# Kernel tuning notes

Hardware: AMD Instinct MI355X
Metric: run time of the kernel (lower is better)

The kernel has to match this reference:

```python
import jax, jax.numpy as jnp
import numpy as np

N = 100000  # nodes
E = 1600000  # edges
D = 128     # hid_dim
LN_EPS = 1e-5


def setup_inputs() -> dict:
    key = jax.random.key(0)
    ks = jax.random.split(key, 14)
    s = 1.0 / np.sqrt(D)
    s2 = 1.0 / np.sqrt(2 * D)
    return {
        "x": jax.random.normal(ks[0], (N, D), jnp.float32),
        "ei": jax.random.randint(ks[1], (2, E), 0, N, dtype=jnp.int32),
        # gin1 mlp: Linear(D,D) + LayerNorm(D)
        "W1": jax.random.normal(ks[2], (D, D), jnp.float32) * s,
        "b1": jnp.zeros((D,), jnp.float32),
        "g1": jnp.ones((D,), jnp.float32),
        "bt1": jnp.zeros((D,), jnp.float32),
        # gin2 mlp
        "W2": jax.random.normal(ks[3], (D, D), jnp.float32) * s,
        "b2": jnp.zeros((D,), jnp.float32),
        "g2": jnp.ones((D,), jnp.float32),
        "bt2": jnp.zeros((D,), jnp.float32),
        # merge MLP: Linear(2D,2D) -> ReLU -> Linear(2D,D) -> ReLU
        "Wl1": jax.random.normal(ks[4], (2 * D, 2 * D), jnp.float32) * s2,
        "bl1": jnp.zeros((2 * D,), jnp.float32),
        "Wl2": jax.random.normal(ks[5], (D, 2 * D), jnp.float32) * s2,
        "bl2": jnp.zeros((D,), jnp.float32),
    }


def _layer_norm(h, g, b):
    mu = jnp.mean(h, axis=-1, keepdims=True)
    var = jnp.mean(jnp.square(h - mu), axis=-1, keepdims=True)
    return (h - mu) * jax.lax.rsqrt(var + LN_EPS) * g + b


def _gin_branch(x, src, dst, W, b, g, beta):
    # GINConv with eps=0: h = x + sum_{(src->dst)} x[src]
    agg = jax.ops.segment_sum(x[src], dst, num_segments=N)
    h = x + agg
    # ResBlock(Linear -> LayerNorm -> ReLU)
    y = jax.nn.relu(_layer_norm(h @ W.T + b, g, beta))
    return h + y


def reference(x, ei, W1, b1, g1, bt1, W2, b2, g2, bt2, Wl1, bl1, Wl2, bl2):
    src, dst = ei[0], ei[1]
    ret1 = _gin_branch(x, src, dst, W1, b1, g1, bt1)        # original edges
    ret2 = _gin_branch(x, dst, src, W2, b2, g2, bt2)        # flipped edges ei[[1,0]]
    cat = jnp.concatenate((ret1, ret2), axis=-1)            # [N, 2D]
    h = jax.nn.relu(cat @ Wl1.T + bl1)
    return jax.nn.relu(h @ Wl2.T + bl2)                     # [N, D]
```

## Files before the change

### kernel.cpp

```cpp
#include <hip/hip_runtime.h>
#include <hip/hip_bf16.h>

#define NN 100000
#define EE 1600000
#define DD 128
#define SCAN_N (2 * NN)
#define SCAN_BLOCKS ((SCAN_N + 1023) / 1024)
#define FILL_PASSES 4
#define FILL_RANGE (NN / FILL_PASSES)

__global__ __launch_bounds__(256) void k_transpose_all(const float* __restrict__ W1,
                                                       const float* __restrict__ W2,
                                                       const float* __restrict__ Wl1,
                                                       const float* __restrict__ Wl2,
                                                       float* __restrict__ Wt1,
                                                       float* __restrict__ Wt2,
                                                       float* __restrict__ Wtl1,
                                                       float* __restrict__ Wtl2) {
    int tid = blockIdx.x * 256 + threadIdx.x;
    const float* in;
    float* out;
    int C, R, off;
    if (tid < 16384)      { in = W1;  out = Wt1;  R = 128; C = 128; off = 0; }
    else if (tid < 32768) { in = W2;  out = Wt2;  R = 128; C = 128; off = 16384; }
    else if (tid < 98304) { in = Wl1; out = Wtl1; R = 256; C = 256; off = 32768; }
    else                  { in = Wl2; out = Wtl2; R = 128; C = 256; off = 98304; }
    int i = tid - off;
    int r = i / C, c = i - r * C;
    out[c * R + r] = in[i];
}

__global__ __launch_bounds__(256) void k_count(const int* __restrict__ ei,
                                               int* __restrict__ off) {
    int e = blockIdx.x * 256 + threadIdx.x;
    int s = ei[e];
    int d = ei[EE + e];
    atomicAdd(&off[d], 1);
    atomicAdd(&off[NN + s], 1);
}

__global__ __launch_bounds__(256) void k_scan1(int* __restrict__ off,
                                               int* __restrict__ bsum) {
    __shared__ int s[256];
    int t = threadIdx.x;
    int base = blockIdx.x * 1024 + t * 4;
    int v[4];
    #pragma unroll
    for (int i = 0; i < 4; ++i) {
        int g = base + i;
        v[i] = (g < SCAN_N) ? off[g] : 0;
    }
    int local = v[0] + v[1] + v[2] + v[3];
    s[t] = local;
    __syncthreads();
    #pragma unroll
    for (int o = 1; o < 256; o <<= 1) {
        int add = (t >= o) ? s[t - o] : 0;
        __syncthreads();
        s[t] += add;
        __syncthreads();
    }
    int run = s[t] - local;
    #pragma unroll
    for (int i = 0; i < 4; ++i) {
        int g = base + i;
        if (g < SCAN_N) off[g] = run;
        run += v[i];
    }
    if (t == 0) bsum[blockIdx.x] = s[255];
}

__global__ __launch_bounds__(256) void k_scan2(int* __restrict__ bsum) {
    __shared__ int s[256];
    int t = threadIdx.x;
    int local = (t < SCAN_BLOCKS) ? bsum[t] : 0;
    s[t] = local;
    __syncthreads();
    #pragma unroll
    for (int o = 1; o < 256; o <<= 1) {
        int add = (t >= o) ? s[t - o] : 0;
        __syncthreads();
        s[t] += add;
        __syncthreads();
    }
    if (t < SCAN_BLOCKS) bsum[t] = s[t] - local;
}

__global__ __launch_bounds__(256) void k_scan3(int* __restrict__ off,
                                               const int* __restrict__ bsum,
                                               int* __restrict__ cur) {
    int t = threadIdx.x;
    int base = blockIdx.x * 1024 + t * 4;
    int add = bsum[blockIdx.x];
    #pragma unroll
    for (int i = 0; i < 4; ++i) {
        int g = base + i;
        if (g < SCAN_N) {
            int v = off[g] + add;
            off[g] = v;
            cur[g] = v;
        }
    }
    if (blockIdx.x == 0 && t == 0) off[SCAN_N] = 2 * EE;
}

__global__ __launch_bounds__(256) void k_fill(const int* __restrict__ ei,
                                              int* __restrict__ cur,
                                              int* __restrict__ idx) {
    int b = blockIdx.x;
    int w = b >> 3, myk = b & 7;
    int e = w * 256 + threadIdx.x;
    int s = ei[e];
    int d = ei[EE + e];
    bool ownD = (((d >> 3) & 7) == myk);
    bool ownS = (((s >> 3) & 7) == myk);
    #pragma unroll
    for (int p = 0; p < FILL_PASSES; ++p) {
        if (ownD && d >= p * FILL_RANGE && d < (p + 1) * FILL_RANGE) {
            int p1 = atomicAdd(&cur[d], 1);
            idx[p1] = s;
        }
        if (ownS && s >= p * FILL_RANGE && s < (p + 1) * FILL_RANGE) {
            int p2 = atomicAdd(&cur[NN + s], 1);
            idx[p2] = d;
        }
        __syncthreads();
    }
}

__global__ __launch_bounds__(256) void k_gather(const float4* __restrict__ x4,
                                                const int* __restrict__ off,
                                                const int* __restrict__ idx,
                                                float4* __restrict__ h1,
                                                float4* __restrict__ h2) {
    int t = threadIdx.x;
    int g = blockIdx.x * 8 + (t >> 5);
    int c = t & 31;
    int n = (g < NN) ? g : g - NN;
    int o0 = off[g], o1 = off[g + 1];
    float4 acc = x4[n * 32 + c];
    int j = o0;
    for (; j + 4 <= o1; j += 4) {
        int n0 = idx[j], n1 = idx[j + 1], n2 = idx[j + 2], n3 = idx[j + 3];
        float4 v0 = x4[n0 * 32 + c];
        float4 v1 = x4[n1 * 32 + c];
        float4 v2 = x4[n2 * 32 + c];
        float4 v3 = x4[n3 * 32 + c];
        acc.x += v0.x + v1.x + v2.x + v3.x;
        acc.y += v0.y + v1.y + v2.y + v3.y;
        acc.z += v0.z + v1.z + v2.z + v3.z;
        acc.w += v0.w + v1.w + v2.w + v3.w;
    }
    for (; j < o1; ++j) {
        int nbr = idx[j];
        float4 v = x4[nbr * 32 + c];
        acc.x += v.x; acc.y += v.y; acc.z += v.z; acc.w += v.w;
    }
    float4* hout = (g < NN) ? h1 : h2;
    hout[n * 32 + c] = acc;
}

__global__ __launch_bounds__(256, 4) void k_branch(const float* __restrict__ h1,
                                                   const float* __restrict__ h2,
                                                   const float* __restrict__ Wt1,
                                                   const float* __restrict__ Wt2,
                                                   const float* __restrict__ bias1,
                                                   const float* __restrict__ bias2,
                                                   const float* __restrict__ gam1,
                                                   const float* __restrict__ gam2,
                                                   const float* __restrict__ beta1,
                                                   const float* __restrict__ beta2,
                                                   float* __restrict__ cat) {
    const int br = blockIdx.y;
    const float* h    = br ? h2    : h1;
    const float* Wt   = br ? Wt2   : Wt1;
    const float* bias = br ? bias2 : bias1;
    const float* gam  = br ? gam2  : gam1;
    const float* beta = br ? beta2 : beta1;
    const int colOff  = br ? 128 : 0;

    __shared__ float hsT[32 * 132];
    __shared__ float wst[32 * 132];
    int t = threadIdx.x;
    int m0 = blockIdx.x * 128;
    int my = t >> 4, tx = t & 15, n0 = tx * 8;

    float acc[8][8];
    #pragma unroll
    for (int i = 0; i < 8; ++i)
        #pragma unroll
        for (int j = 0; j < 8; ++j) acc[i][j] = 0.f;

    for (int k0 = 0; k0 < 128; k0 += 32) {
        __syncthreads();
        #pragma unroll
        for (int it = 0; it < 4; ++it) {
            int f = it * 256 + t;
            int row = f >> 3, q = f & 7;
            int node = m0 + row;
            float4 v = make_float4(0.f, 0.f, 0.f, 0.f);
            if (node < NN) v = ((const float4*)h)[node * 32 + (k0 >> 2) + q];
            hsT[(q * 4 + 0) * 132 + row] = v.x;
            hsT[(q * 4 + 1) * 132 + row] = v.y;
            hsT[(q * 4 + 2) * 132 + row] = v.z;
            hsT[(q * 4 + 3) * 132 + row] = v.w;
        }
        #pragma unroll
        for (int it = 0; it < 4; ++it) {
            int f = it * 256 + t;
            int kl = f >> 5, n4 = f & 31;
            *(float4*)&wst[kl * 132 + n4 * 4] = ((const float4*)Wt)[(k0 + kl) * 32 + n4];
        }
        __syncthreads();
        #pragma unroll 4
        for (int kl = 0; kl < 32; ++kl) {
            float4 a0 = *(const float4*)&hsT[kl * 132 + my * 8];
            float4 a1 = *(const float4*)&hsT[kl * 132 + my * 8 + 4];
            float4 b0 = *(const float4*)&wst[kl * 132 + n0];
            float4 b1 = *(const float4*)&wst[kl * 132 + n0 + 4];
            float aa[8] = {a0.x, a0.y, a0.z, a0.w, a1.x, a1.y, a1.z, a1.w};
            float bb[8] = {b0.x, b0.y, b0.z, b0.w, b1.x, b1.y, b1.z, b1.w};
            #pragma unroll
            for (int i = 0; i < 8; ++i)
                #pragma unroll
                for (int j = 0; j < 8; ++j) acc[i][j] += aa[i] * bb[j];
        }
    }

    float breg[8], greg[8], btreg[8];
    #pragma unroll
    for (int j = 0; j < 8; ++j) {
        breg[j]  = bias[n0 + j];
        greg[j]  = gam[n0 + j];
        btreg[j] = beta[n0 + j];
    }
    #pragma unroll
    for (int i = 0; i < 8; ++i) {
        float s = 0.f, q = 0.f;
        #pragma unroll
        for (int j = 0; j < 8; ++j) {
            float v = acc[i][j] + breg[j];
            acc[i][j] = v;
            s += v;
            q += v * v;
        }
        #pragma unroll
        for (int o = 1; o < 16; o <<= 1) {
            s += __shfl_xor(s, o);
            q += __shfl_xor(q, o);
        }
        float mu  = s * (1.f / 128.f);
        float var = q * (1.f / 128.f) - mu * mu;
        float rs  = rsqrtf(var + 1e-5f);
        int node = m0 + my * 8 + i;
        if (node < NN) {
            const float4* hrow = (const float4*)&h[(size_t)node * 128];
            float4 r0 = hrow[tx * 2];
            float4 r1 = hrow[tx * 2 + 1];
            float hres[8] = {r0.x, r0.y, r0.z, r0.w, r1.x, r1.y, r1.z, r1.w};
            float o_[8];
            #pragma unroll
            for (int j = 0; j < 8; ++j) {
                float y = (acc[i][j] - mu) * rs * greg[j] + btreg[j];
                o_[j] = hres[j] + fmaxf(y, 0.f);
            }
            float4* cp = (float4*)&cat[(size_t)node * 256 + colOff + n0];
            cp[0] = make_float4(o_[0], o_[1], o_[2], o_[3]);
            cp[1] = make_float4(o_[4], o_[5], o_[6], o_[7]);
        }
    }
}

__global__ __launch_bounds__(256, 4) void k_mlp1(const float* __restrict__ cat,
                                                 const float* __restrict__ Wt,
                                                 const float* __restrict__ bias,
                                                 float* __restrict__ mid) {
    __shared__ float hsT[32 * 132];
    __shared__ float wst[32 * 132];
    int t = threadIdx.x;
    int m0 = blockIdx.x * 128;
    int nbase = blockIdx.y * 128;
    int my = t >> 4, tx = t & 15, n0 = tx * 8;

    float acc[8][8];
    #pragma unroll
    for (int i = 0; i < 8; ++i)
        #pragma unroll
        for (int j = 0; j < 8; ++j) acc[i][j] = 0.f;

    for (int k0 = 0; k0 < 256; k0 += 32) {
        __syncthreads();
        #pragma unroll
        for (int it = 0; it < 4; ++it) {
            int f = it * 256 + t;
            int row = f >> 3, q = f & 7;
            int node = m0 + row;
            float4 v = make_float4(0.f, 0.f, 0.f, 0.f);
            if (node < NN) v = ((const float4*)cat)[(size_t)node * 64 + (k0 >> 2) + q];
            hsT[(q * 4 + 0) * 132 + row] = v.x;
            hsT[(q * 4 + 1) * 132 + row] = v.y;
            hsT[(q * 4 + 2) * 132 + row] = v.z;
            hsT[(q * 4 + 3) * 132 + row] = v.w;
        }
        #pragma unroll
        for (int it = 0; it < 4; ++it) {
            int f = it * 256 + t;
            int kl = f >> 5, n4 = f & 31;
            *(float4*)&wst[kl * 132 + n4 * 4] =
                ((const float4*)Wt)[(k0 + kl) * 64 + blockIdx.y * 32 + n4];
        }
        __syncthreads();
        #pragma unroll 4
        for (int kl = 0; kl < 32; ++kl) {
            float4 a0 = *(const float4*)&hsT[kl * 132 + my * 8];
            float4 a1 = *(const float4*)&hsT[kl * 132 + my * 8 + 4];
            float4 b0 = *(const float4*)&wst[kl * 132 + n0];
            float4 b1 = *(const float4*)&wst[kl * 132 + n0 + 4];
            float aa[8] = {a0.x, a0.y, a0.z, a0.w, a1.x, a1.y, a1.z, a1.w};
            float bb[8] = {b0.x, b0.y, b0.z, b0.w, b1.x, b1.y, b1.z, b1.w};
            #pragma unroll
            for (int i = 0; i < 8; ++i)
                #pragma unroll
                for (int j = 0; j < 8; ++j) acc[i][j] += aa[i] * bb[j];
        }
    }

    float breg[8];
    #pragma unroll
    for (int j = 0; j < 8; ++j) breg[j] = bias[nbase + n0 + j];
    #pragma unroll
    for (int i = 0; i < 8; ++i) {
        int node = m0 + my * 8 + i;
        if (node < NN) {
            float o_[8];
            #pragma unroll
            for (int j = 0; j < 8; ++j) o_[j] = fmaxf(acc[i][j] + breg[j], 0.f);
            float4* mp = (float4*)&mid[(size_t)node * 256 + nbase + n0];
            mp[0] = make_float4(o_[0], o_[1], o_[2], o_[3]);
            mp[1] = make_float4(o_[4], o_[5], o_[6], o_[7]);
        }
    }
}

__global__ __launch_bounds__(256, 4) void k_mlp2(const float* __restrict__ mid,
                                                 const float* __restrict__ Wt,
                                                 const float* __restrict__ bias,
                                                 float* __restrict__ out) {
    __shared__ float hsT[32 * 132];
    __shared__ float wst[32 * 132];
    int t = threadIdx.x;
    int m0 = blockIdx.x * 128;
    int my = t >> 4, tx = t & 15, n0 = tx * 8;

    float acc[8][8];
    #pragma unroll
    for (int i = 0; i < 8; ++i)
        #pragma unroll
        for (int j = 0; j < 8; ++j) acc[i][j] = 0.f;

    for (int k0 = 0; k0 < 256; k0 += 32) {
        __syncthreads();
        #pragma unroll
        for (int it = 0; it < 4; ++it) {
            int f = it * 256 + t;
            int row = f >> 3, q = f & 7;
            int node = m0 + row;
            float4 v = make_float4(0.f, 0.f, 0.f, 0.f);
            if (node < NN) v = ((const float4*)mid)[(size_t)node * 64 + (k0 >> 2) + q];
            hsT[(q * 4 + 0) * 132 + row] = v.x;
            hsT[(q * 4 + 1) * 132 + row] = v.y;
            hsT[(q * 4 + 2) * 132 + row] = v.z;
            hsT[(q * 4 + 3) * 132 + row] = v.w;
        }
        #pragma unroll
        for (int it = 0; it < 4; ++it) {
            int f = it * 256 + t;
            int kl = f >> 5, n4 = f & 31;
            *(float4*)&wst[kl * 132 + n4 * 4] = ((const float4*)Wt)[(k0 + kl) * 32 + n4];
        }
        __syncthreads();
        #pragma unroll 4
        for (int kl = 0; kl < 32; ++kl) {
            float4 a0 = *(const float4*)&hsT[kl * 132 + my * 8];
            float4 a1 = *(const float4*)&hsT[kl * 132 + my * 8 + 4];
            float4 b0 = *(const float4*)&wst[kl * 132 + n0];
            float4 b1 = *(const float4*)&wst[kl * 132 + n0 + 4];
            float aa[8] = {a0.x, a0.y, a0.z, a0.w, a1.x, a1.y, a1.z, a1.w};
            float bb[8] = {b0.x, b0.y, b0.z, b0.w, b1.x, b1.y, b1.z, b1.w};
            #pragma unroll
            for (int i = 0; i < 8; ++i)
                #pragma unroll
                for (int j = 0; j < 8; ++j) acc[i][j] += aa[i] * bb[j];
        }
    }

    float breg[8];
    #pragma unroll
    for (int j = 0; j < 8; ++j) breg[j] = bias[n0 + j];
    #pragma unroll
    for (int i = 0; i < 8; ++i) {
        int node = m0 + my * 8 + i;
        if (node < NN) {
            float o_[8];
            #pragma unroll
            for (int j = 0; j < 8; ++j) o_[j] = fmaxf(acc[i][j] + breg[j], 0.f);
            float4* op = (float4*)&out[(size_t)node * 128 + n0];
            op[0] = make_float4(o_[0], o_[1], o_[2], o_[3]);
            op[1] = make_float4(o_[4], o_[5], o_[6], o_[7]);
        }
    }
}

extern "C" void kernel_launch(void* const* d_in, const int* in_sizes, int n_in,
                              void* d_out, int out_size, void* d_ws, size_t ws_size,
                              hipStream_t stream) {
    const float* x   = (const float*)d_in[0];
    const int*   ei  = (const int*)d_in[1];
    const float* W1  = (const float*)d_in[2];
    const float* b1  = (const float*)d_in[3];
    const float* g1  = (const float*)d_in[4];
    const float* bt1 = (const float*)d_in[5];
    const float* W2  = (const float*)d_in[6];
    const float* b2  = (const float*)d_in[7];
    const float* g2  = (const float*)d_in[8];
    const float* bt2 = (const float*)d_in[9];
    const float* Wl1 = (const float*)d_in[10];
    const float* bl1 = (const float*)d_in[11];
    const float* Wl2 = (const float*)d_in[12];
    const float* bl2 = (const float*)d_in[13];
    float* out = (float*)d_out;

    float* ws   = (float*)d_ws;
    float* h1   = ws;
    float* h2   = ws + (size_t)NN * DD;
    float* mid  = ws;
    float* cat  = ws + (size_t)2 * NN * DD;
    float* Wt1  = ws + (size_t)4 * NN * DD;
    float* Wt2  = Wt1 + 128 * 128;
    float* Wtl1 = Wt2 + 128 * 128;
    float* Wtl2 = Wtl1 + 256 * 256;
    int*   off  = (int*)(Wtl2 + 128 * 256);
    int*   cur  = off + SCAN_N + 1;
    int*   idx  = cur + SCAN_N;
    int*   bsum = idx + 2 * EE;

    k_transpose_all<<<512, 256, 0, stream>>>(W1, W2, Wl1, Wl2, Wt1, Wt2, Wtl1, Wtl2);

    hipMemsetAsync(off, 0, (SCAN_N + 1) * sizeof(int), stream);
    k_count<<<EE / 256, 256, 0, stream>>>(ei, off);
    k_scan1<<<SCAN_BLOCKS, 256, 0, stream>>>(off, bsum);
    k_scan2<<<1, 256, 0, stream>>>(bsum);
    k_scan3<<<SCAN_BLOCKS, 256, 0, stream>>>(off, bsum, cur);
    k_fill<<<(EE / 256) * 8, 256, 0, stream>>>(ei, cur, idx);

    k_gather<<<SCAN_N / 8, 256, 0, stream>>>((const float4*)x, off, idx,
                                             (float4*)h1, (float4*)h2);

    int nb128 = (NN + 127) / 128;
    k_branch<<<dim3(nb128, 2), 256, 0, stream>>>(h1, h2, Wt1, Wt2,
                                                 b1, b2, g1, g2, bt1, bt2, cat);
    k_mlp1<<<dim3(nb128, 2), 256, 0, stream>>>(cat, Wtl1, bl1, mid);
    k_mlp2<<<nb128, 256, 0, stream>>>(mid, Wtl2, bl2, out);
}
```

Measured before the change: 980.5 us.

## Run merge MLP GEMMs on MFMA with split-bf16 (3-pass) emulation of fp32

```diff
diff --git a/kernel.cpp b/kernel.cpp
--- a/kernel.cpp
+++ b/kernel.cpp
@@ -9,25 +9,43 @@
 #define FILL_PASSES 4
 #define FILL_RANGE (NN / FILL_PASSES)
 
-__global__ __launch_bounds__(256) void k_transpose_all(const float* __restrict__ W1,
-                                                       const float* __restrict__ W2,
-                                                       const float* __restrict__ Wl1,
-                                                       const float* __restrict__ Wl2,
-                                                       float* __restrict__ Wt1,
-                                                       float* __restrict__ Wt2,
-                                                       float* __restrict__ Wtl1,
-                                                       float* __restrict__ Wtl2) {
+typedef unsigned short u16;
+typedef __attribute__((ext_vector_type(8))) short short8v;
+typedef __attribute__((ext_vector_type(4))) float f32x4;
+
+__device__ inline void bf16split(float v, u16& hi, u16& lo) {
+    __hip_bfloat16 h = __float2bfloat16(v);
+    hi = *reinterpret_cast<u16*>(&h);
+    float r = v - __bfloat162float(h);
+    __hip_bfloat16 l = __float2bfloat16(r);
+    lo = *reinterpret_cast<u16*>(&l);
+}
+
+__global__ __launch_bounds__(256) void k_prep(const float* __restrict__ W1,
+                                              const float* __restrict__ W2,
+                                              const float* __restrict__ Wl1,
+                                              const float* __restrict__ Wl2,
+                                              float* __restrict__ Wt1,
+                                              float* __restrict__ Wt2,
+                                              u16* __restrict__ Wl1hi,
+                                              u16* __restrict__ Wl1lo,
+                                              u16* __restrict__ Wl2hi,
+                                              u16* __restrict__ Wl2lo) {
     int tid = blockIdx.x * 256 + threadIdx.x;
-    const float* in;
-    float* out;
-    int C, R, off;
-    if (tid < 16384)      { in = W1;  out = Wt1;  R = 128; C = 128; off = 0; }
-    else if (tid < 32768) { in = W2;  out = Wt2;  R = 128; C = 128; off = 16384; }
-    else if (tid < 98304) { in = Wl1; out = Wtl1; R = 256; C = 256; off = 32768; }
-    else                  { in = Wl2; out = Wtl2; R = 128; C = 256; off = 98304; }
-    int i = tid - off;
-    int r = i / C, c = i - r * C;
-    out[c * R + r] = in[i];
+    if (tid < 16384) {
+        int r = tid >> 7, c = tid & 127;
+        Wt1[c * 128 + r] = W1[tid];
+    } else if (tid < 32768) {
+        int i = tid - 16384;
+        int r = i >> 7, c = i & 127;
+        Wt2[c * 128 + r] = W2[i];
+    } else if (tid < 98304) {
+        int i = tid - 32768;
+        bf16split(Wl1[i], Wl1hi[i], Wl1lo[i]);
+    } else {
+        int i = tid - 98304;
+        bf16split(Wl2[i], Wl2hi[i], Wl2lo[i]);
+    }
 }
 
 __global__ __launch_bounds__(256) void k_count(const int* __restrict__ ei,
@@ -271,142 +289,94 @@
     }
 }
 
-__global__ __launch_bounds__(256, 4) void k_mlp1(const float* __restrict__ cat,
-                                                 const float* __restrict__ Wt,
-                                                 const float* __restrict__ bias,
-                                                 float* __restrict__ mid) {
-    __shared__ float hsT[32 * 132];
-    __shared__ float wst[32 * 132];
+__global__ __launch_bounds__(256, 2) void k_mfma_mlp(const float* __restrict__ A,
+                                                     const u16* __restrict__ Bhi,
+                                                     const u16* __restrict__ Blo,
+                                                     const float* __restrict__ bias,
+                                                     float* __restrict__ C,
+                                                     int ldC) {
+    __shared__ u16 ahi[128 * 40], alo[128 * 40], bhi[128 * 40], blo[128 * 40];
     int t = threadIdx.x;
     int m0 = blockIdx.x * 128;
     int nbase = blockIdx.y * 128;
-    int my = t >> 4, tx = t & 15, n0 = tx * 8;
-
-    float acc[8][8];
-    #pragma unroll
-    for (int i = 0; i < 8; ++i)
-        #pragma unroll
-        for (int j = 0; j < 8; ++j) acc[i][j] = 0.f;
+    int lane = t & 63, wid = t >> 6;
+    int wm = wid >> 1, wn = wid & 1;
+    int lr = lane & 15, lg = lane >> 4;
+
+    f32x4 acc[4][4];
+    #pragma unroll
+    for (int i = 0; i < 4; ++i)
+        #pragma unroll
+        for (int j = 0; j < 4; ++j) acc[i][j] = (f32x4){0.f, 0.f, 0.f, 0.f};
 
     for (int k0 = 0; k0 < 256; k0 += 32) {
         __syncthreads();
         #pragma unroll
         for (int it = 0; it < 4; ++it) {
             int f = it * 256 + t;
-            int row = f >> 3, q = f & 7;
-            int node = m0 + row;
+            int m = f >> 3, q = f & 7;
+            int node = m0 + m;
             float4 v = make_float4(0.f, 0.f, 0.f, 0.f);
-            if (node < NN) v = ((const float4*)cat)[(size_t)node * 64 + (k0 >> 2) + q];
-            hsT[(q * 4 + 0) * 132 + row] = v.x;
-            hsT[(q * 4 + 1) * 132 + row] = v.y;
-            hsT[(q * 4 + 2) * 132 + row] = v.z;
-            hsT[(q * 4 + 3) * 132 + row] = v.w;
-        }
-        #pragma unroll
-        for (int it = 0; it < 4; ++it) {
+            if (node < NN) v = ((const float4*)A)[(size_t)node * 64 + (k0 >> 2) + q];
+            u16 h0, l0, h1_, l1_, h2_, l2_, h3, l3;
+            bf16split(v.x, h0, l0);
+            bf16split(v.y, h1_, l1_);
+            bf16split(v.z, h2_, l2_);
+            bf16split(v.w, h3, l3);
+            uint* ph = (uint*)&ahi[m * 40 + q * 4];
+            ph[0] = (uint)h0 | ((uint)h1_ << 16);
+            ph[1] = (uint)h2_ | ((uint)h3 << 16);
+            uint* pl = (uint*)&alo[m * 40 + q * 4];
+            pl[0] = (uint)l0 | ((uint)l1_ << 16);
+            pl[1] = (uint)l2_ | ((uint)l3 << 16);
+        }
+        #pragma unroll
+        for (int it = 0; it < 2; ++it) {
             int f = it * 256 + t;
-            int kl = f >> 5, n4 = f & 31;
-            *(float4*)&wst[kl * 132 + n4 * 4] =
-                ((const float4*)Wt)[(k0 + kl) * 64 + blockIdx.y * 32 + n4];
-        }
-        __syncthreads();
-        #pragma unroll 4
-        for (int kl = 0; kl < 32; ++kl) {
-            float4 a0 = *(const float4*)&hsT[kl * 132 + my * 8];
-            float4 a1 = *(const float4*)&hsT[kl * 132 + my * 8 + 4];
-            float4 b0 = *(const float4*)&wst[kl * 132 + n0];
-            float4 b1 = *(const float4*)&wst[kl * 132 + n0 + 4];
-            float aa[8] = {a0.x, a0.y, a0.z, a0.w, a1.x, a1.y, a1.z, a1.w};
-            float bb[8] = {b0.x, b0.y, b0.z, b0.w, b1.x, b1.y, b1.z, b1.w};
+            int n = f >> 2, q = f & 3;
+            size_t gsrc = (size_t)(nbase + n) * 256 + k0 + q * 8;
+            uint4 vh = *(const uint4*)&Bhi[gsrc];
+            uint4 vl = *(const uint4*)&Blo[gsrc];
+            *(uint4*)&bhi[n * 40 + q * 8] = vh;
+            *(uint4*)&blo[n * 40 + q * 8] = vl;
+        }
+        __syncthreads();
+
+        short8v afh[4], afl[4];
+        #pragma unroll
+        for (int mt = 0; mt < 4; ++mt) {
+            int r = wm * 64 + mt * 16 + lr;
+            afh[mt] = *(const short8v*)&ahi[r * 40 + lg * 8];
+            afl[mt] = *(const short8v*)&alo[r * 40 + lg * 8];
+        }
+        #pragma unroll
+        for (int nt = 0; nt < 4; ++nt) {
+            int c = wn * 64 + nt * 16 + lr;
+            short8v bfh = *(const short8v*)&bhi[c * 40 + lg * 8];
+            short8v bfl = *(const short8v*)&blo[c * 40 + lg * 8];
             #pragma unroll
-            for (int i = 0; i < 8; ++i)
-                #pragma unroll
-                for (int j = 0; j < 8; ++j) acc[i][j] += aa[i] * bb[j];
-        }
-    }
-
-    float breg[8];
-    #pragma unroll
-    for (int j = 0; j < 8; ++j) breg[j] = bias[nbase + n0 + j];
-    #pragma unroll
-    for (int i = 0; i < 8; ++i) {
-        int node = m0 + my * 8 + i;
-        if (node < NN) {
-            float o_[8];
+            for (int mt = 0; mt < 4; ++mt) {
+                acc[mt][nt] = __builtin_amdgcn_mfma_f32_16x16x32_bf16(afh[mt], bfh, acc[mt][nt], 0, 0, 0);
+                acc[mt][nt] = __builtin_amdgcn_mfma_f32_16x16x32_bf16(afh[mt], bfl, acc[mt][nt], 0, 0, 0);
+                acc[mt][nt] = __builtin_amdgcn_mfma_f32_16x16x32_bf16(afl[mt], bfh, acc[mt][nt], 0, 0, 0);
+            }
+        }
+    }
+
+    #pragma unroll
+    for (int nt = 0; nt < 4; ++nt) {
+        int col = nbase + wn * 64 + nt * 16 + lr;
+        float bv = bias[col];
+        #pragma unroll
+        for (int mt = 0; mt < 4; ++mt) {
             #pragma unroll
-            for (int j = 0; j < 8; ++j) o_[j] = fmaxf(acc[i][j] + breg[j], 0.f);
-            float4* mp = (float4*)&mid[(size_t)node * 256 + nbase + n0];
-            mp[0] = make_float4(o_[0], o_[1], o_[2], o_[3]);
-            mp[1] = make_float4(o_[4], o_[5], o_[6], o_[7]);
-        }
-    }
-}
-
-__global__ __launch_bounds__(256, 4) void k_mlp2(const float* __restrict__ mid,
-                                                 const float* __restrict__ Wt,
-                                                 const float* __restrict__ bias,
-                                                 float* __restrict__ out) {
-    __shared__ float hsT[32 * 132];
-    __shared__ float wst[32 * 132];
-    int t = threadIdx.x;
-    int m0 = blockIdx.x * 128;
-    int my = t >> 4, tx = t & 15, n0 = tx * 8;
-
-    float acc[8][8];
-    #pragma unroll
-    for (int i = 0; i < 8; ++i)
-        #pragma unroll
-        for (int j = 0; j < 8; ++j) acc[i][j] = 0.f;
-
-    for (int k0 = 0; k0 < 256; k0 += 32) {
-        __syncthreads();
-        #pragma unroll
-        for (int it = 0; it < 4; ++it) {
-            int f = it * 256 + t;
-            int row = f >> 3, q = f & 7;
-            int node = m0 + row;
-            float4 v = make_float4(0.f, 0.f, 0.f, 0.f);
-            if (node < NN) v = ((const float4*)mid)[(size_t)node * 64 + (k0 >> 2) + q];
-            hsT[(q * 4 + 0) * 132 + row] = v.x;
-            hsT[(q * 4 + 1) * 132 + row] = v.y;
-            hsT[(q * 4 + 2) * 132 + row] = v.z;
-            hsT[(q * 4 + 3) * 132 + row] = v.w;
-        }
-        #pragma unroll
-        for (int it = 0; it < 4; ++it) {
-            int f = it * 256 + t;
-            int kl = f >> 5, n4 = f & 31;
-            *(float4*)&wst[kl * 132 + n4 * 4] = ((const float4*)Wt)[(k0 + kl) * 32 + n4];
-        }
-        __syncthreads();
-        #pragma unroll 4
-        for (int kl = 0; kl < 32; ++kl) {
-            float4 a0 = *(const float4*)&hsT[kl * 132 + my * 8];
-            float4 a1 = *(const float4*)&hsT[kl * 132 + my * 8 + 4];
-            float4 b0 = *(const float4*)&wst[kl * 132 + n0];
-            float4 b1 = *(const float4*)&wst[kl * 132 + n0 + 4];
-            float aa[8] = {a0.x, a0.y, a0.z, a0.w, a1.x, a1.y, a1.z, a1.w};
-            float bb[8] = {b0.x, b0.y, b0.z, b0.w, b1.x, b1.y, b1.z, b1.w};
-            #pragma unroll
-            for (int i = 0; i < 8; ++i)
-                #pragma unroll
-                for (int j = 0; j < 8; ++j) acc[i][j] += aa[i] * bb[j];
-        }
-    }
-
-    float breg[8];
-    #pragma unroll
-    for (int j = 0; j < 8; ++j) breg[j] = bias[n0 + j];
-    #pragma unroll
-    for (int i = 0; i < 8; ++i) {
-        int node = m0 + my * 8 + i;
-        if (node < NN) {
-            float o_[8];
-            #pragma unroll
-            for (int j = 0; j < 8; ++j) o_[j] = fmaxf(acc[i][j] + breg[j], 0.f);
-            float4* op = (float4*)&out[(size_t)node * 128 + n0];
-            op[0] = make_float4(o_[0], o_[1], o_[2], o_[3]);
-            op[1] = make_float4(o_[4], o_[5], o_[6], o_[7]);
+            for (int r = 0; r < 4; ++r) {
+                int row = m0 + wm * 64 + mt * 16 + lg * 4 + r;
+                if (row < NN) {
+                    float v = fmaxf(acc[mt][nt][r] + bv, 0.f);
+                    C[(size_t)row * ldC + col] = v;
+                }
+            }
         }
     }
 }
@@ -430,21 +400,24 @@
     const float* bl2 = (const float*)d_in[13];
     float* out = (float*)d_out;
 
-    float* ws   = (float*)d_ws;
-    float* h1   = ws;
-    float* h2   = ws + (size_t)NN * DD;
-    float* mid  = ws;
-    float* cat  = ws + (size_t)2 * NN * DD;
-    float* Wt1  = ws + (size_t)4 * NN * DD;
-    float* Wt2  = Wt1 + 128 * 128;
-    float* Wtl1 = Wt2 + 128 * 128;
-    float* Wtl2 = Wtl1 + 256 * 256;
-    int*   off  = (int*)(Wtl2 + 128 * 256);
-    int*   cur  = off + SCAN_N + 1;
-    int*   idx  = cur + SCAN_N;
-    int*   bsum = idx + 2 * EE;
-
-    k_transpose_all<<<512, 256, 0, stream>>>(W1, W2, Wl1, Wl2, Wt1, Wt2, Wtl1, Wtl2);
+    float* ws    = (float*)d_ws;
+    float* h1    = ws;
+    float* h2    = ws + (size_t)NN * DD;
+    float* mid   = ws;
+    float* cat   = ws + (size_t)2 * NN * DD;
+    float* Wt1   = ws + (size_t)4 * NN * DD;
+    float* Wt2   = Wt1 + 128 * 128;
+    u16*   Wl1hi = (u16*)(Wt2 + 128 * 128);
+    u16*   Wl1lo = Wl1hi + 256 * 256;
+    u16*   Wl2hi = Wl1lo + 256 * 256;
+    u16*   Wl2lo = Wl2hi + 128 * 256;
+    int*   off   = (int*)(Wl2lo + 128 * 256);
+    int*   cur   = off + SCAN_N + 1;
+    int*   idx   = cur + SCAN_N;
+    int*   bsum  = idx + 2 * EE;
+
+    k_prep<<<512, 256, 0, stream>>>(W1, W2, Wl1, Wl2, Wt1, Wt2,
+                                    Wl1hi, Wl1lo, Wl2hi, Wl2lo);
 
     hipMemsetAsync(off, 0, (SCAN_N + 1) * sizeof(int), stream);
     k_count<<<EE / 256, 256, 0, stream>>>(ei, off);
@@ -459,6 +432,7 @@
     int nb128 = (NN + 127) / 128;
     k_branch<<<dim3(nb128, 2), 256, 0, stream>>>(h1, h2, Wt1, Wt2,
                                                  b1, b2, g1, g2, bt1, bt2, cat);
-    k_mlp1<<<dim3(nb128, 2), 256, 0, stream>>>(cat, Wtl1, bl1, mid);
-    k_mlp2<<<nb128, 256, 0, stream>>>(mid, Wtl2, bl2, out);
-}
+
+    k_mfma_mlp<<<dim3(nb128, 2), 256, 0, stream>>>(cat, Wl1hi, Wl1lo, bl1, mid, 256);
+    k_mfma_mlp<<<dim3(nb128, 1), 256, 0, stream>>>(mid, Wl2hi, Wl2lo, bl2, out, 128);
+}
```

Result: faster. 868.8 us (-11.4%).
